# Kernel optimization log

Hardware: AMD Instinct MI355X
Metric: run time of the kernel (lower is better)

## Reference

```python
import jax, jax.numpy as jnp
import numpy as np

B, N, C = 64, 256, 512
SHIFTS = (-1, 0, 1)
# torch.chunk(N, 3): ceil(256/3)=86 -> sizes [86, 86, 84]
CHUNK_SIZES = (86, 86, 84)
EPS = 1e-5


def _shift_pad(a, s):
    # shift along last axis (C) with zero padding, matching shift_with_padding
    if s == 0:
        return a
    if s > 0:
        return jnp.pad(a[..., :-s], ((0, 0), (0, 0), (s, 0)))
    s = -s
    return jnp.pad(a[..., s:], ((0, 0), (0, 0), (0, s)))


def setup_inputs() -> dict:
    key = jax.random.key(0)
    ks = jax.random.split(key, 16)
    w = lambda k, shape: (jax.random.normal(k, shape, jnp.float32) * 0.02)
    inp = {
        "x": jax.random.normal(ks[0], (B, N, C), jnp.float32),
        "ln_g": jnp.ones((C,), jnp.float32),
        "ln_b": jnp.zeros((C,), jnp.float32),
        "Ws": w(ks[1], (C, C)),
        "bs": jnp.zeros((C,), jnp.float32),
        "Wc": w(ks[2], (N, N, 3)),     # Conv1d weight [out=N, in=N, k=3]
        "bc": jnp.zeros((N,), jnp.float32),
        "We1": w(ks[3], (N, N // 8)),
        "be1": jnp.zeros((N // 8,), jnp.float32),
        "We2": w(ks[4], (N // 8, N)),
        "be2": jnp.zeros((N,), jnp.float32),
        "Wf1": w(ks[5], (C, 2 * C)),
        "bf1": jnp.zeros((2 * C,), jnp.float32),
        "Wf2": w(ks[6], (2 * C, C)),
        "bf2": jnp.zeros((C,), jnp.float32),
    }
    return inp


def reference(x, ln_g, ln_b, Ws, bs, Wc, bc, We1, be1, We2, be2, Wf1, bf1, Wf2, bf2):
    res = x
    # channel_mixer_S: LayerNorm over C, then Linear C->C + relu (dropout=0)
    mu = jnp.mean(x, axis=-1, keepdims=True)
    var = jnp.mean((x - mu) ** 2, axis=-1, keepdims=True)
    h = (x - mu) * jax.lax.rsqrt(var + EPS) * ln_g + ln_b
    h = jax.nn.relu(h @ Ws + bs)                      # [B, N, C]
    # channel_shift: chunk along N, shift each chunk along C with zero pad
    offs = np.cumsum((0,) + CHUNK_SIZES)
    chunks = [h[:, offs[i]:offs[i + 1], :] for i in range(3)]
    x_shift = jnp.concatenate([_shift_pad(c, s) for c, s in zip(chunks, SHIFTS)], axis=1)
    # channel_projection: Conv1d over C with N channels, k=3, pad=1
    x_shift = jax.lax.conv_general_dilated(
        x_shift, Wc, window_strides=(1,), padding=[(1, 1)],
        dimension_numbers=("NCH", "OIH", "NCH")) + bc[None, :, None]
    # SE gating
    se = jnp.mean(x_shift, axis=-1)                   # [B, N]
    ex = jax.nn.sigmoid(jax.nn.relu(se @ We1 + be1) @ We2 + be2)  # [B, N]
    z = x_shift * ex[:, :, None]
    # channel_mixer_F: C -> 2C (relu) -> C, residual
    z = jax.nn.relu(z @ Wf1 + bf1) @ Wf2 + bf2 + res
    return z
```

## Files before the change

kernel.cpp:

```cpp
#include <hip/hip_runtime.h>
#include <hip/hip_bf16.h>
#include <math.h>

#define BB 64
#define NN 256
#define CCH 512

typedef unsigned short u16;
typedef __attribute__((ext_vector_type(8))) short s16x8;
typedef __attribute__((ext_vector_type(4))) float f32x4;

#define AS1 __attribute__((address_space(1)))
#define AS3 __attribute__((address_space(3)))

static __device__ __forceinline__ float b2f(u16 u) {
    union { unsigned int i; float f; } x; x.i = ((unsigned int)u) << 16; return x.f;
}
static __device__ __forceinline__ u16 f2b(float f) {
    __hip_bfloat16 h = __float2bfloat16(f);
    union { __hip_bfloat16 h; u16 u; } x; x.h = h; return x.u;
}
static __device__ __forceinline__ void gll16(const void* g, void* l) {
    __builtin_amdgcn_global_load_lds((const AS1 unsigned int*)g,
                                     (AS3 unsigned int*)l, 16, 0, 0);
}

#define VM6  asm volatile("s_waitcnt vmcnt(6)" ::: "memory")
#define VM3  asm volatile("s_waitcnt vmcnt(3)" ::: "memory")
#define VM0  asm volatile("s_waitcnt vmcnt(0)" ::: "memory")
#define MEMB asm volatile("" ::: "memory")

__global__ __launch_bounds__(256) void ln_kernel(const float* __restrict__ x,
    const float* __restrict__ g, const float* __restrict__ bta,
    u16* __restrict__ out)
{
    const int l = threadIdx.x & 63;
    const int r = blockIdx.x * 4 + (threadIdx.x >> 6);
    const float4* xr = (const float4*)(x + (size_t)r * CCH);
    float4 v1 = xr[l];
    float4 v2 = xr[l + 64];
    float s  = v1.x + v1.y + v1.z + v1.w + v2.x + v2.y + v2.z + v2.w;
    float ss = v1.x*v1.x + v1.y*v1.y + v1.z*v1.z + v1.w*v1.w
             + v2.x*v2.x + v2.y*v2.y + v2.z*v2.z + v2.w*v2.w;
    #pragma unroll
    for (int o = 32; o > 0; o >>= 1) {
        s  += __shfl_xor(s, o);
        ss += __shfl_xor(ss, o);
    }
    float mu  = s * (1.0f / CCH);
    float var = ss * (1.0f / CCH) - mu * mu;
    float rs  = rsqrtf(var + 1e-5f);
    float4 g1 = ((const float4*)g)[l],      g2 = ((const float4*)g)[l + 64];
    float4 b1 = ((const float4*)bta)[l],    b2 = ((const float4*)bta)[l + 64];
    ushort4 o1, o2;
    o1.x = f2b((v1.x - mu) * rs * g1.x + b1.x);
    o1.y = f2b((v1.y - mu) * rs * g1.y + b1.y);
    o1.z = f2b((v1.z - mu) * rs * g1.z + b1.z);
    o1.w = f2b((v1.w - mu) * rs * g1.w + b1.w);
    o2.x = f2b((v2.x - mu) * rs * g2.x + b2.x);
    o2.y = f2b((v2.y - mu) * rs * g2.y + b2.y);
    o2.z = f2b((v2.z - mu) * rs * g2.z + b2.z);
    o2.w = f2b((v2.w - mu) * rs * g2.w + b2.w);
    ushort4* orow = (ushort4*)(out + (size_t)r * CCH);
    orow[l]      = o1;
    orow[l + 64] = o2;
}

static __device__ __forceinline__ void wtc_body(const float* __restrict__ W,
    u16* __restrict__ Wt, int K, int N, int bx, int by, float* t )
{
    int n0 = bx * 32, k0 = by * 32;
    int tx = threadIdx.x & 31, ty = threadIdx.x >> 5;
    #pragma unroll
    for (int i = 0; i < 4; ++i)
        t[(ty + i * 8) * 33 + tx] = W[(size_t)(k0 + ty + i * 8) * N + n0 + tx];
    __syncthreads();
    #pragma unroll
    for (int i = 0; i < 4; ++i)
        Wt[(size_t)(n0 + ty + i * 8) * K + k0 + tx] = f2b(t[tx * 33 + ty + i * 8]);
}

__global__ __launch_bounds__(256) void prep_kernel(
    const float* __restrict__ Ws,  u16* __restrict__ Wst,
    const float* __restrict__ Wf1, u16* __restrict__ Wf1t,
    const float* __restrict__ Wf2, u16* __restrict__ Wf2t,
    const float* __restrict__ Wc,  u16* __restrict__ Wc3,
    u16* __restrict__ Hts, float* __restrict__ SEraw)
{
    __shared__ float t[32 * 33];
    int bid = blockIdx.x;
    if (bid < 256) {
        wtc_body(Ws, Wst, 512, 512, bid & 15, bid >> 4, t);
    } else if (bid < 768) {
        int idx = bid - 256;
        wtc_body(Wf1, Wf1t, 512, 1024, idx & 31, idx >> 5, t);
    } else if (bid < 1280) {
        int idx = bid - 768;
        wtc_body(Wf2, Wf2t, 1024, 512, idx & 15, idx >> 4, t);
    } else if (bid < 2048) {
        int idx = (bid - 1280) * 256 + threadIdx.x;
        int i = idx & 255;
        int o = (idx >> 8) & 255;
        int k = idx >> 16;
        Wc3[idx] = f2b(Wc[((size_t)o * NN + i) * 3 + k]);
    } else {
        int idx = (bid - 2048) * 256 + threadIdx.x;
        if (idx < 65536) {
            int b   = idx >> 10;
            int rem = idx & 1023;
            int rr  = rem >> 8;
            int r   = (rr & 1) + (rr >> 1) * 512;
            Hts[((size_t)b * 514 + r) * 256 + (rem & 255)] = 0;
        } else {
            SEraw[idx - 65536] = 0.0f;
        }
    }
}

template<int MODE>
__global__ __launch_bounds__(512, 1) void gemm_pipe(
    const u16* __restrict__ A, const u16* __restrict__ Bt,
    const float* __restrict__ bias, const float* __restrict__ scale,
    const float* __restrict__ res, void* __restrict__ outv,
    u16* __restrict__ auxout, float* __restrict__ SEraw)
{
    constexpr int NK = (MODE == 2) ? 32 : (MODE == 3) ? 24 : 16;
    constexpr int SA = (MODE == 2) ? 1024 : 512;
    constexpr int SB = (MODE == 2) ? 1024 : 512;
    constexpr int NOUT = (MODE == 1) ? 1024 : 512;

    __shared__ u16 Asm[4 * 256 * 32];
    __shared__ u16 Bsm[4 * 128 * 32];

    const int tid = threadIdx.x;
    const int l   = tid & 63;
    const int w   = tid >> 6;
    const int nwg = gridDim.x;
    const int work = (blockIdx.x & 7) * (nwg >> 3) + (blockIdx.x >> 3);

    int row0, col0, bidx = 0;
    if (MODE == 0)      { row0 = (work >> 7) * 256; col0 = (work & 127) * 128; }
    else if (MODE == 1) { row0 = (work >> 3) * 256; col0 = (work & 7) * 128; }
    else if (MODE == 2) { row0 = (work >> 2) * 256; col0 = (work & 3) * 128; }
    else                { row0 = 0; bidx = work >> 2; col0 = (work & 3) * 128; }

    const u16* Aab  = A + (size_t)row0 * SA;
    const u16* Bab  = Bt + (size_t)col0 * SB;
    const u16* HtsB = Bt + (size_t)bidx * 514 * 256;

    const int wm = (w >> 2) * 128;
    const int wn = (w & 3) * 32;
    const int fr = l & 15;
    const int q  = l >> 4;
    const int kofs = ((q ^ ((l >> 1) & 3)) * 8);

    const f32x4 zero = {0.0f, 0.0f, 0.0f, 0.0f};
    f32x4 acc[8][2];
    #pragma unroll
    for (int m = 0; m < 8; ++m) { acc[m][0] = zero; acc[m][1] = zero; }

    const int kc0 = ((tid & 3) ^ ((tid >> 3) & 3)) * 8;
    const int srow = tid >> 2;

    auto stage = [&](int u) {
        const int slot = u & 3;
        u16* ald = Asm + slot * 8192 + w * 512;
        u16* bld = Bsm + slot * 4096 + w * 512;
        if (MODE == 3) {
            const int kseg = u >> 3, kb = (u & 7) * 32 + kc0;
            gll16(A + kseg * 65536 + srow * 256 + kb, ald);
            gll16(A + kseg * 65536 + (srow + 128) * 256 + kb, ald + 4096);
            gll16(HtsB + (size_t)(col0 + srow + kseg) * 256 + kb, bld);
        } else {
            const int kb = u * 32 + kc0;
            gll16(Aab + (size_t)srow * SA + kb, ald);
            gll16(Aab + (size_t)(srow + 128) * SA + kb, ald + 4096);
            gll16(Bab + (size_t)srow * SB + kb, bld);
        }
    };

    stage(0); stage(1); stage(2);

    for (int u = 0; u < NK; ++u) {
        if (u < NK - 2)       { VM6; }
        else if (u == NK - 2) { VM3; }
        else                  { VM0; }
        __builtin_amdgcn_s_barrier();
        MEMB;
        const int slot = u & 3;
        s16x8 bf0  = *(const s16x8*)&Bsm[slot * 4096 + (wn + fr) * 32 + kofs];
        s16x8 bf1v = *(const s16x8*)&Bsm[slot * 4096 + (wn + 16 + fr) * 32 + kofs];
        s16x8 af[8];
        #pragma unroll
        for (int m = 0; m < 8; ++m)
            af[m] = *(const s16x8*)&Asm[slot * 8192 + (wm + m * 16 + fr) * 32 + kofs];
        if (u + 3 < NK) stage(u + 3);
        __builtin_amdgcn_s_setprio(1);
        #pragma unroll
        for (int m = 0; m < 8; ++m) {
            acc[m][0] = __builtin_amdgcn_mfma_f32_16x16x32_bf16(af[m], bf0,  acc[m][0], 0, 0, 0);
            acc[m][1] = __builtin_amdgcn_mfma_f32_16x16x32_bf16(af[m], bf1v, acc[m][1], 0, 0, 0);
        }
        __builtin_amdgcn_s_setprio(0);
        MEMB;
    }

    if (MODE == 0) {
        #pragma unroll
        for (int m = 0; m < 8; ++m) {
            #pragma unroll
            for (int j = 0; j < 4; ++j) {
                const int c = row0 + wm + m * 16 + (l >> 4) * 4 + j;
                const float bsv = bias[c];
                #pragma unroll
                for (int n = 0; n < 2; ++n) {
                    const int gcol = col0 + wn + n * 16 + fr;
                    const int b  = gcol >> 8;
                    const int ni = gcol & 255;
                    const int s  = (ni < 86) ? -1 : (ni < 172 ? 0 : 1);
                    auxout[((size_t)b * 514 + c + 1 + s) * 256 + ni] =
                        f2b(fmaxf(acc[m][n][j] + bsv, 0.0f));
                }
            }
        }
    } else if (MODE == 1) {
        #pragma unroll
        for (int m = 0; m < 8; ++m) {
            #pragma unroll
            for (int j = 0; j < 4; ++j) {
                const int row = row0 + wm + m * 16 + (l >> 4) * 4 + j;
                const float sc = scale[row];
                #pragma unroll
                for (int n = 0; n < 2; ++n) {
                    const int col = col0 + wn + n * 16 + fr;
                    ((u16*)outv)[(size_t)row * NOUT + col] =
                        f2b(fmaxf(acc[m][n][j] * sc + bias[col], 0.0f));
                }
            }
        }
    } else if (MODE == 2) {
        #pragma unroll
        for (int m = 0; m < 8; ++m) {
            #pragma unroll
            for (int j = 0; j < 4; ++j) {
                const int row = row0 + wm + m * 16 + (l >> 4) * 4 + j;
                #pragma unroll
                for (int n = 0; n < 2; ++n) {
                    const int col = col0 + wn + n * 16 + fr;
                    ((float*)outv)[(size_t)row * NOUT + col] =
                        acc[m][n][j] + bias[col] + res[(size_t)row * NOUT + col];
                }
            }
        }
    } else {
        #pragma unroll
        for (int m = 0; m < 8; ++m) {
            #pragma unroll
            for (int j = 0; j < 4; ++j) {
                const int no = wm + m * 16 + (l >> 4) * 4 + j;
                const float bcv = bias[no];
                float p = 0.0f;
                #pragma unroll
                for (int n = 0; n < 2; ++n) {
                    const int c = col0 + wn + n * 16 + fr;
                    float v = acc[m][n][j];
                    auxout[((size_t)bidx * NN + no) * CCH + c] = f2b(v + bcv);
                    p += v;
                }
                p += __shfl_xor(p, 1);
                p += __shfl_xor(p, 2);
                p += __shfl_xor(p, 4);
                p += __shfl_xor(p, 8);
                if (fr == 0) atomicAdd(&SEraw[bidx * NN + no], p);
            }
        }
    }
}

__global__ __launch_bounds__(256) void semlp_kernel(const float* __restrict__ seraw,
    const float* __restrict__ bc,
    const float* __restrict__ We1, const float* __restrict__ be1,
    const float* __restrict__ We2, const float* __restrict__ be2,
    float* __restrict__ ex)
{
    __shared__ float sse[256];
    __shared__ float e1[32];
    int b = blockIdx.x, t = threadIdx.x;
    sse[t] = seraw[b * 256 + t] * (1.0f / CCH) + bc[t];
    __syncthreads();
    if (t < 32) {
        float a = be1[t];
        #pragma unroll 8
        for (int i = 0; i < 256; ++i) a += sse[i] * We1[i * 32 + t];
        e1[t] = fmaxf(a, 0.0f);
    }
    __syncthreads();
    float a = be2[t];
    #pragma unroll
    for (int j = 0; j < 32; ++j) a += e1[j] * We2[j * 256 + t];
    ex[b * 256 + t] = 1.0f / (1.0f + expf(-a));
}

extern "C" void kernel_launch(void* const* d_in, const int* in_sizes, int n_in,
                              void* d_out, int out_size, void* d_ws, size_t ws_size,
                              hipStream_t stream) {
    const float* x    = (const float*)d_in[0];
    const float* ln_g = (const float*)d_in[1];
    const float* ln_b = (const float*)d_in[2];
    const float* Ws   = (const float*)d_in[3];
    const float* bs   = (const float*)d_in[4];
    const float* Wc   = (const float*)d_in[5];
    const float* bc   = (const float*)d_in[6];
    const float* We1  = (const float*)d_in[7];
    const float* be1  = (const float*)d_in[8];
    const float* We2  = (const float*)d_in[9];
    const float* be2  = (const float*)d_in[10];
    const float* Wf1  = (const float*)d_in[11];
    const float* bf1  = (const float*)d_in[12];
    const float* Wf2  = (const float*)d_in[13];
    const float* bf2  = (const float*)d_in[14];
    float* out = (float*)d_out;
    char* w8   = (char*)d_ws;

    u16* XN  = (u16*)(w8);
    u16* Y   = XN;
    u16* Hts = (u16*)(w8 + (16u << 20));
    u16* T   = (u16*)(w8 + (16u << 20));
    char* tail = w8 + 50397184;
    float* SEraw = (float*)(tail);
    float* EX    = (float*)(tail + 65536);
    u16* Wst     = (u16*)(tail + 131072);
    u16* Wf1t    = (u16*)(tail + 655360);
    u16* Wf2t    = (u16*)(tail + 1703936);
    u16* Wc3     = (u16*)(tail + 2752512);

    prep_kernel<<<2368, 256, 0, stream>>>(Ws, Wst, Wf1, Wf1t, Wf2, Wf2t,
                                          Wc, Wc3, Hts, SEraw);
    ln_kernel<<<BB * NN / 4, 256, 0, stream>>>(x, ln_g, ln_b, XN);
    gemm_pipe<0><<<256, 512, 0, stream>>>(Wst, XN, bs, nullptr, nullptr,
                                          nullptr, Hts, nullptr);
    gemm_pipe<3><<<256, 512, 0, stream>>>(Wc3, Hts, bc, nullptr, nullptr,
                                          nullptr, Y, SEraw);
    semlp_kernel<<<BB, 256, 0, stream>>>(SEraw, bc, We1, be1, We2, be2, EX);
    gemm_pipe<1><<<512, 512, 0, stream>>>(Y, Wf1t, bf1, EX, nullptr,
                                          T, nullptr, nullptr);
    gemm_pipe<2><<<256, 512, 0, stream>>>(T, Wf2t, bf2, nullptr, x,
                                          out, nullptr, nullptr);
}
```

Measured before the change: 129.5 us.

## Fuse LayerNorm into prep, widen FFN1 GEMM tile, replace SE atomics with partials

The LayerNorm kernel is folded into the weight-prep kernel, which removes one launch. The first FFN GEMM now uses 256x256 output tiles (256 workgroups instead of 512), which raises reuse of the A operand per load at the cost of more accumulator registers and deeper vmcnt waits. The SE-sum atomicAdds and their zero-initialisation are replaced by per-column-tile partial writes that semlp_kernel sums. The larger tile halves the number of workgroups, which could reduce load balance across CUs.

Result: faster. 115.4 us (-10.9%).

```diff
diff --git a/kernel.cpp b/kernel.cpp
--- a/kernel.cpp
+++ b/kernel.cpp
@@ -13,9 +13,6 @@
 #define AS1 __attribute__((address_space(1)))
 #define AS3 __attribute__((address_space(3)))
 
-static __device__ __forceinline__ float b2f(u16 u) {
-    union { unsigned int i; float f; } x; x.i = ((unsigned int)u) << 16; return x.f;
-}
 static __device__ __forceinline__ u16 f2b(float f) {
     __hip_bfloat16 h = __float2bfloat16(f);
     union { __hip_bfloat16 h; u16 u; } x; x.h = h; return x.u;
@@ -25,46 +22,12 @@
                                      (AS3 unsigned int*)l, 16, 0, 0);
 }
 
+#define VM8  asm volatile("s_waitcnt vmcnt(8)" ::: "memory")
 #define VM6  asm volatile("s_waitcnt vmcnt(6)" ::: "memory")
+#define VM4  asm volatile("s_waitcnt vmcnt(4)" ::: "memory")
 #define VM3  asm volatile("s_waitcnt vmcnt(3)" ::: "memory")
 #define VM0  asm volatile("s_waitcnt vmcnt(0)" ::: "memory")
 #define MEMB asm volatile("" ::: "memory")
-
-__global__ __launch_bounds__(256) void ln_kernel(const float* __restrict__ x,
-    const float* __restrict__ g, const float* __restrict__ bta,
-    u16* __restrict__ out)
-{
-    const int l = threadIdx.x & 63;
-    const int r = blockIdx.x * 4 + (threadIdx.x >> 6);
-    const float4* xr = (const float4*)(x + (size_t)r * CCH);
-    float4 v1 = xr[l];
-    float4 v2 = xr[l + 64];
-    float s  = v1.x + v1.y + v1.z + v1.w + v2.x + v2.y + v2.z + v2.w;
-    float ss = v1.x*v1.x + v1.y*v1.y + v1.z*v1.z + v1.w*v1.w
-             + v2.x*v2.x + v2.y*v2.y + v2.z*v2.z + v2.w*v2.w;
-    #pragma unroll
-    for (int o = 32; o > 0; o >>= 1) {
-        s  += __shfl_xor(s, o);
-        ss += __shfl_xor(ss, o);
-    }
-    float mu  = s * (1.0f / CCH);
-    float var = ss * (1.0f / CCH) - mu * mu;
-    float rs  = rsqrtf(var + 1e-5f);
-    float4 g1 = ((const float4*)g)[l],      g2 = ((const float4*)g)[l + 64];
-    float4 b1 = ((const float4*)bta)[l],    b2 = ((const float4*)bta)[l + 64];
-    ushort4 o1, o2;
-    o1.x = f2b((v1.x - mu) * rs * g1.x + b1.x);
-    o1.y = f2b((v1.y - mu) * rs * g1.y + b1.y);
-    o1.z = f2b((v1.z - mu) * rs * g1.z + b1.z);
-    o1.w = f2b((v1.w - mu) * rs * g1.w + b1.w);
-    o2.x = f2b((v2.x - mu) * rs * g2.x + b2.x);
-    o2.y = f2b((v2.y - mu) * rs * g2.y + b2.y);
-    o2.z = f2b((v2.z - mu) * rs * g2.z + b2.z);
-    o2.w = f2b((v2.w - mu) * rs * g2.w + b2.w);
-    ushort4* orow = (ushort4*)(out + (size_t)r * CCH);
-    orow[l]      = o1;
-    orow[l + 64] = o2;
-}
 
 static __device__ __forceinline__ void wtc_body(const float* __restrict__ W,
     u16* __restrict__ Wt, int K, int N, int bx, int by, float* t )
@@ -80,12 +43,14 @@
         Wt[(size_t)(n0 + ty + i * 8) * K + k0 + tx] = f2b(t[tx * 33 + ty + i * 8]);
 }
 
-__global__ __launch_bounds__(256) void prep_kernel(
+__global__ __launch_bounds__(256) void prep_ln_kernel(
     const float* __restrict__ Ws,  u16* __restrict__ Wst,
     const float* __restrict__ Wf1, u16* __restrict__ Wf1t,
     const float* __restrict__ Wf2, u16* __restrict__ Wf2t,
     const float* __restrict__ Wc,  u16* __restrict__ Wc3,
-    u16* __restrict__ Hts, float* __restrict__ SEraw)
+    u16* __restrict__ Hts,
+    const float* __restrict__ x, const float* __restrict__ g,
+    const float* __restrict__ bta, u16* __restrict__ xnorm)
 {
     __shared__ float t[32 * 33];
     int bid = blockIdx.x;
@@ -103,34 +68,63 @@
         int o = (idx >> 8) & 255;
         int k = idx >> 16;
         Wc3[idx] = f2b(Wc[((size_t)o * NN + i) * 3 + k]);
+    } else if (bid < 2304) {
+        int idx = (bid - 2048) * 256 + threadIdx.x;
+        int b   = idx >> 10;
+        int rem = idx & 1023;
+        int rr  = rem >> 8;
+        int r   = (rr & 1) + (rr >> 1) * 512;
+        Hts[((size_t)b * 514 + r) * 256 + (rem & 255)] = 0;
     } else {
-        int idx = (bid - 2048) * 256 + threadIdx.x;
-        if (idx < 65536) {
-            int b   = idx >> 10;
-            int rem = idx & 1023;
-            int rr  = rem >> 8;
-            int r   = (rr & 1) + (rr >> 1) * 512;
-            Hts[((size_t)b * 514 + r) * 256 + (rem & 255)] = 0;
-        } else {
-            SEraw[idx - 65536] = 0.0f;
-        }
+        const int l = threadIdx.x & 63;
+        const int r = (bid - 2304) * 4 + (threadIdx.x >> 6);
+        const float4* xr = (const float4*)(x + (size_t)r * CCH);
+        float4 v1 = xr[l];
+        float4 v2 = xr[l + 64];
+        float s  = v1.x + v1.y + v1.z + v1.w + v2.x + v2.y + v2.z + v2.w;
+        float ss = v1.x*v1.x + v1.y*v1.y + v1.z*v1.z + v1.w*v1.w
+                 + v2.x*v2.x + v2.y*v2.y + v2.z*v2.z + v2.w*v2.w;
+        #pragma unroll
+        for (int o = 32; o > 0; o >>= 1) {
+            s  += __shfl_xor(s, o);
+            ss += __shfl_xor(ss, o);
+        }
+        float mu  = s * (1.0f / CCH);
+        float var = ss * (1.0f / CCH) - mu * mu;
+        float rs  = rsqrtf(var + 1e-5f);
+        float4 g1 = ((const float4*)g)[l],   g2 = ((const float4*)g)[l + 64];
+        float4 b1 = ((const float4*)bta)[l], b2 = ((const float4*)bta)[l + 64];
+        ushort4 o1, o2;
+        o1.x = f2b((v1.x - mu) * rs * g1.x + b1.x);
+        o1.y = f2b((v1.y - mu) * rs * g1.y + b1.y);
+        o1.z = f2b((v1.z - mu) * rs * g1.z + b1.z);
+        o1.w = f2b((v1.w - mu) * rs * g1.w + b1.w);
+        o2.x = f2b((v2.x - mu) * rs * g2.x + b2.x);
+        o2.y = f2b((v2.y - mu) * rs * g2.y + b2.y);
+        o2.z = f2b((v2.z - mu) * rs * g2.z + b2.z);
+        o2.w = f2b((v2.w - mu) * rs * g2.w + b2.w);
+        ushort4* orow = (ushort4*)(xnorm + (size_t)r * CCH);
+        orow[l]      = o1;
+        orow[l + 64] = o2;
     }
 }
 
-template<int MODE>
+template<int MODE, int BNT>
 __global__ __launch_bounds__(512, 1) void gemm_pipe(
     const u16* __restrict__ A, const u16* __restrict__ Bt,
     const float* __restrict__ bias, const float* __restrict__ scale,
     const float* __restrict__ res, void* __restrict__ outv,
-    u16* __restrict__ auxout, float* __restrict__ SEraw)
+    u16* __restrict__ auxout, float* __restrict__ SEpart)
 {
     constexpr int NK = (MODE == 2) ? 32 : (MODE == 3) ? 24 : 16;
     constexpr int SA = (MODE == 2) ? 1024 : 512;
     constexpr int SB = (MODE == 2) ? 1024 : 512;
     constexpr int NOUT = (MODE == 1) ? 1024 : 512;
+    constexpr int NF = BNT / 64;
+    constexpr int BSZ = BNT * 32;
 
     __shared__ u16 Asm[4 * 256 * 32];
-    __shared__ u16 Bsm[4 * 128 * 32];
+    __shared__ u16 Bsm[4 * BSZ];
 
     const int tid = threadIdx.x;
     const int l   = tid & 63;
@@ -140,7 +134,7 @@
 
     int row0, col0, bidx = 0;
     if (MODE == 0)      { row0 = (work >> 7) * 256; col0 = (work & 127) * 128; }
-    else if (MODE == 1) { row0 = (work >> 3) * 256; col0 = (work & 7) * 128; }
+    else if (MODE == 1) { row0 = (work >> 2) * 256; col0 = (work & 3) * 256; }
     else if (MODE == 2) { row0 = (work >> 2) * 256; col0 = (work & 3) * 128; }
     else                { row0 = 0; bidx = work >> 2; col0 = (work & 3) * 128; }
 
@@ -149,15 +143,17 @@
     const u16* HtsB = Bt + (size_t)bidx * 514 * 256;
 
     const int wm = (w >> 2) * 128;
-    const int wn = (w & 3) * 32;
+    const int wn = (w & 3) * (BNT / 4);
     const int fr = l & 15;
     const int q  = l >> 4;
     const int kofs = ((q ^ ((l >> 1) & 3)) * 8);
 
     const f32x4 zero = {0.0f, 0.0f, 0.0f, 0.0f};
-    f32x4 acc[8][2];
+    f32x4 acc[8][NF];
     #pragma unroll
-    for (int m = 0; m < 8; ++m) { acc[m][0] = zero; acc[m][1] = zero; }
+    for (int m = 0; m < 8; ++m)
+        #pragma unroll
+        for (int n = 0; n < NF; ++n) acc[m][n] = zero;
 
     const int kc0 = ((tid & 3) ^ ((tid >> 3) & 3)) * 8;
     const int srow = tid >> 2;
@@ -165,7 +161,7 @@
     auto stage = [&](int u) {
         const int slot = u & 3;
         u16* ald = Asm + slot * 8192 + w * 512;
-        u16* bld = Bsm + slot * 4096 + w * 512;
+        u16* bld = Bsm + slot * BSZ + w * 512;
         if (MODE == 3) {
             const int kseg = u >> 3, kb = (u & 7) * 32 + kc0;
             gll16(A + kseg * 65536 + srow * 256 + kb, ald);
@@ -176,20 +172,30 @@
             gll16(Aab + (size_t)srow * SA + kb, ald);
             gll16(Aab + (size_t)(srow + 128) * SA + kb, ald + 4096);
             gll16(Bab + (size_t)srow * SB + kb, bld);
+            if (BNT == 256)
+                gll16(Bab + (size_t)(srow + 128) * SB + kb, bld + 4096);
         }
     };
 
     stage(0); stage(1); stage(2);
 
     for (int u = 0; u < NK; ++u) {
-        if (u < NK - 2)       { VM6; }
-        else if (u == NK - 2) { VM3; }
-        else                  { VM0; }
+        if (BNT == 128) {
+            if (u < NK - 2)       { VM6; }
+            else if (u == NK - 2) { VM3; }
+            else                  { VM0; }
+        } else {
+            if (u < NK - 2)       { VM8; }
+            else if (u == NK - 2) { VM4; }
+            else                  { VM0; }
+        }
         __builtin_amdgcn_s_barrier();
         MEMB;
         const int slot = u & 3;
-        s16x8 bf0  = *(const s16x8*)&Bsm[slot * 4096 + (wn + fr) * 32 + kofs];
-        s16x8 bf1v = *(const s16x8*)&Bsm[slot * 4096 + (wn + 16 + fr) * 32 + kofs];
+        s16x8 bfv[NF];
+        #pragma unroll
+        for (int n = 0; n < NF; ++n)
+            bfv[n] = *(const s16x8*)&Bsm[slot * BSZ + (wn + n * 16 + fr) * 32 + kofs];
         s16x8 af[8];
         #pragma unroll
         for (int m = 0; m < 8; ++m)
@@ -197,10 +203,10 @@
         if (u + 3 < NK) stage(u + 3);
         __builtin_amdgcn_s_setprio(1);
         #pragma unroll
-        for (int m = 0; m < 8; ++m) {
-            acc[m][0] = __builtin_amdgcn_mfma_f32_16x16x32_bf16(af[m], bf0,  acc[m][0], 0, 0, 0);
-            acc[m][1] = __builtin_amdgcn_mfma_f32_16x16x32_bf16(af[m], bf1v, acc[m][1], 0, 0, 0);
-        }
+        for (int m = 0; m < 8; ++m)
+            #pragma unroll
+            for (int n = 0; n < NF; ++n)
+                acc[m][n] = __builtin_amdgcn_mfma_f32_16x16x32_bf16(af[m], bfv[n], acc[m][n], 0, 0, 0);
         __builtin_amdgcn_s_setprio(0);
         MEMB;
     }
@@ -213,7 +219,7 @@
                 const int c = row0 + wm + m * 16 + (l >> 4) * 4 + j;
                 const float bsv = bias[c];
                 #pragma unroll
-                for (int n = 0; n < 2; ++n) {
+                for (int n = 0; n < NF; ++n) {
                     const int gcol = col0 + wn + n * 16 + fr;
                     const int b  = gcol >> 8;
                     const int ni = gcol & 255;
@@ -231,7 +237,7 @@
                 const int row = row0 + wm + m * 16 + (l >> 4) * 4 + j;
                 const float sc = scale[row];
                 #pragma unroll
-                for (int n = 0; n < 2; ++n) {
+                for (int n = 0; n < NF; ++n) {
                     const int col = col0 + wn + n * 16 + fr;
                     ((u16*)outv)[(size_t)row * NOUT + col] =
                         f2b(fmaxf(acc[m][n][j] * sc + bias[col], 0.0f));
@@ -245,7 +251,7 @@
             for (int j = 0; j < 4; ++j) {
                 const int row = row0 + wm + m * 16 + (l >> 4) * 4 + j;
                 #pragma unroll
-                for (int n = 0; n < 2; ++n) {
+                for (int n = 0; n < NF; ++n) {
                     const int col = col0 + wn + n * 16 + fr;
                     ((float*)outv)[(size_t)row * NOUT + col] =
                         acc[m][n][j] + bias[col] + res[(size_t)row * NOUT + col];
@@ -253,6 +259,7 @@
             }
         }
     } else {
+        const int ct = col0 >> 7;
         #pragma unroll
         for (int m = 0; m < 8; ++m) {
             #pragma unroll
@@ -261,7 +268,7 @@
                 const float bcv = bias[no];
                 float p = 0.0f;
                 #pragma unroll
-                for (int n = 0; n < 2; ++n) {
+                for (int n = 0; n < NF; ++n) {
                     const int c = col0 + wn + n * 16 + fr;
                     float v = acc[m][n][j];
                     auxout[((size_t)bidx * NN + no) * CCH + c] = f2b(v + bcv);
@@ -271,13 +278,14 @@
                 p += __shfl_xor(p, 2);
                 p += __shfl_xor(p, 4);
                 p += __shfl_xor(p, 8);
-                if (fr == 0) atomicAdd(&SEraw[bidx * NN + no], p);
+                if (fr == 0)
+                    SEpart[ct * 16384 + bidx * NN + no] = p;
             }
         }
     }
 }
 
-__global__ __launch_bounds__(256) void semlp_kernel(const float* __restrict__ seraw,
+__global__ __launch_bounds__(256) void semlp_kernel(const float* __restrict__ sep,
     const float* __restrict__ bc,
     const float* __restrict__ We1, const float* __restrict__ be1,
     const float* __restrict__ We2, const float* __restrict__ be2,
@@ -286,7 +294,9 @@
     __shared__ float sse[256];
     __shared__ float e1[32];
     int b = blockIdx.x, t = threadIdx.x;
-    sse[t] = seraw[b * 256 + t] * (1.0f / CCH) + bc[t];
+    int o = b * 256 + t;
+    sse[t] = (sep[o] + sep[16384 + o] + sep[32768 + o] + sep[49152 + o])
+             * (1.0f / CCH) + bc[t];
     __syncthreads();
     if (t < 32) {
         float a = be1[t];
@@ -327,23 +337,22 @@
     u16* Hts = (u16*)(w8 + (16u << 20));
     u16* T   = (u16*)(w8 + (16u << 20));
     char* tail = w8 + 50397184;
-    float* SEraw = (float*)(tail);
-    float* EX    = (float*)(tail + 65536);
-    u16* Wst     = (u16*)(tail + 131072);
-    u16* Wf1t    = (u16*)(tail + 655360);
-    u16* Wf2t    = (u16*)(tail + 1703936);
-    u16* Wc3     = (u16*)(tail + 2752512);
-
-    prep_kernel<<<2368, 256, 0, stream>>>(Ws, Wst, Wf1, Wf1t, Wf2, Wf2t,
-                                          Wc, Wc3, Hts, SEraw);
-    ln_kernel<<<BB * NN / 4, 256, 0, stream>>>(x, ln_g, ln_b, XN);
-    gemm_pipe<0><<<256, 512, 0, stream>>>(Wst, XN, bs, nullptr, nullptr,
-                                          nullptr, Hts, nullptr);
-    gemm_pipe<3><<<256, 512, 0, stream>>>(Wc3, Hts, bc, nullptr, nullptr,
-                                          nullptr, Y, SEraw);
-    semlp_kernel<<<BB, 256, 0, stream>>>(SEraw, bc, We1, be1, We2, be2, EX);
-    gemm_pipe<1><<<512, 512, 0, stream>>>(Y, Wf1t, bf1, EX, nullptr,
-                                          T, nullptr, nullptr);
-    gemm_pipe<2><<<256, 512, 0, stream>>>(T, Wf2t, bf2, nullptr, x,
-                                          out, nullptr, nullptr);
-}
+    float* SEpart = (float*)(tail);
+    float* EX     = (float*)(tail + 262144);
+    u16* Wst      = (u16*)(tail + 327680);
+    u16* Wf1t     = (u16*)(tail + 851968);
+    u16* Wf2t     = (u16*)(tail + 1900544);
+    u16* Wc3      = (u16*)(tail + 2949120);
+
+    prep_ln_kernel<<<6400, 256, 0, stream>>>(Ws, Wst, Wf1, Wf1t, Wf2, Wf2t,
+                                             Wc, Wc3, Hts, x, ln_g, ln_b, XN);
+    gemm_pipe<0, 128><<<256, 512, 0, stream>>>(Wst, XN, bs, nullptr, nullptr,
+                                               nullptr, Hts, nullptr);
+    gemm_pipe<3, 128><<<256, 512, 0, stream>>>(Wc3, Hts, bc, nullptr, nullptr,
+                                               nullptr, Y, SEpart);
+    semlp_kernel<<<BB, 256, 0, stream>>>(SEpart, bc, We1, be1, We2, be2, EX);
+    gemm_pipe<1, 256><<<256, 512, 0, stream>>>(Y, Wf1t, bf1, EX, nullptr,
+                                               T, nullptr, nullptr);
+    gemm_pipe<2, 128><<<256, 512, 0, stream>>>(T, Wf2t, bf2, nullptr, x,
+                                               out, nullptr, nullptr);
+}
```
